# Kernel tuning notes

Hardware: AMD Instinct MI355X
Metric: run time of the kernel (lower is better)

The kernel has to match this reference:

```python
import jax, jax.numpy as jnp
import numpy as np


def setup_inputs() -> dict:
    key = jax.random.key(0)
    kq, kk, kv = jax.random.split(key, 3)
    B, L, Q, H, E = 8, 128, 8, 8, 64
    S, P = 128, 8
    queries = jax.random.normal(kq, (B, L, Q, H, E), dtype=jnp.float32)
    keys = jax.random.normal(kk, (B, S, P, H, E), dtype=jnp.float32)
    values = jax.random.normal(kv, (B, S, P, H, E), dtype=jnp.float32)
    attn_mask = jnp.zeros((1,), dtype=bool)  # unused by the module
    return {"queries": queries, "keys": keys, "values": values, "attn_mask": attn_mask}


def reference(queries, keys, values, attn_mask):
    # queries: [B,L,Q,H,E]; keys/values: [B,S,P,H,E]
    B, L, Q, H, E = queries.shape
    S, P = values.shape[1], values.shape[2]
    scale = 1.0 / np.sqrt(E).astype(np.float32)
    # scores: [B,S,P,L,Q,H]
    scores = jnp.einsum('blqhe,bsphe->bsplqh', queries, keys)
    # softmax over joint (S,P) axis
    scaled = (scale * scores).reshape(B, S * P, L, Q, H)
    attn = jax.nn.softmax(scaled, axis=1).reshape(B, S, P, L, Q, H)
    # dropout is identity in eval / with p=0.0
    V = jnp.einsum('bsphe,bsplqh->blqhe', values, attn)
    return V
```

## Files before the change

kernel.cpp:

```cpp
#include <hip/hip_runtime.h>
#include <hip/hip_bf16.h>

typedef __attribute__((ext_vector_type(4))) float f32x4;
typedef __attribute__((ext_vector_type(16))) float f32x16;
typedef __attribute__((ext_vector_type(8))) short bf16x8;
typedef __attribute__((ext_vector_type(4))) unsigned u32x4;

#define MFMA32(a, b, c) __builtin_amdgcn_mfma_f32_32x32x16_bf16(a, b, c, 0, 0, 0)
#define EXP2(x) __builtin_amdgcn_exp2f(x)

constexpr int Bc = 8, Hc = 8;
constexpr int NQ = 1024;
constexpr int NK = 1024;
constexpr int RS = 512;
constexpr int Ec = 64;
constexpr int KT = 128;
constexpr int NT = NK / KT;
constexpr float QSCALE2 = 0.125f * 1.4426950408889634f;
constexpr float DEFER_THR = 8.0f;

__device__ __forceinline__ short f2bf(float x) {
    return (short)__builtin_bit_cast(unsigned short, __float2bfloat16(x));
}

__device__ __forceinline__ bf16x8 pack2(float4 a, float4 b) {
    bf16x8 r;
    r[0] = f2bf(a.x); r[1] = f2bf(a.y); r[2] = f2bf(a.z); r[3] = f2bf(a.w);
    r[4] = f2bf(b.x); r[5] = f2bf(b.y); r[6] = f2bf(b.z); r[7] = f2bf(b.w);
    return r;
}

__device__ __forceinline__ bf16x8 pack2s(float4 a, float4 b, float s) {
    bf16x8 r;
    r[0] = f2bf(a.x * s); r[1] = f2bf(a.y * s); r[2] = f2bf(a.z * s); r[3] = f2bf(a.w * s);
    r[4] = f2bf(b.x * s); r[5] = f2bf(b.y * s); r[6] = f2bf(b.z * s); r[7] = f2bf(b.w * s);
    return r;
}

__device__ __forceinline__ unsigned cvtpk(float a, float b) {
    unsigned lo = (unsigned short)__builtin_bit_cast(unsigned short, __float2bfloat16(a));
    unsigned hi = (unsigned short)__builtin_bit_cast(unsigned short, __float2bfloat16(b));
    return lo | (hi << 16);
}

__device__ __forceinline__ void gload16(const short* src, short* dst) {
    __builtin_amdgcn_global_load_lds((const __attribute__((address_space(1))) void*)src,
                                     (__attribute__((address_space(3))) void*)dst, 16, 0, 0);
}

__global__ __launch_bounds__(256, 4)
void cvt_kv(const float* __restrict__ Kg, const float* __restrict__ Vg,
            short* __restrict__ Kbf, short* __restrict__ Vt) {
    __shared__ __attribute__((aligned(16))) short Vl[64][72];
    const int tid  = threadIdx.x;
    const int head = blockIdx.x >> 4;
    const int kb   = blockIdx.x & 15;
    const int b    = head >> 3, h = head & 7;
    const int row  = tid >> 2, q = tid & 3;

    const size_t gin = (((size_t)(b * NK + kb * 64 + row)) * 8 + h) * 64 + q * 16;
    const float4* kp = (const float4*)(Kg + gin);
    float4 k0 = kp[0], k1 = kp[1], k2 = kp[2], k3 = kp[3];
    short* kout = Kbf + ((size_t)head * NK + kb * 64 + row) * 64 + q * 16;
    ((bf16x8*)kout)[0] = pack2(k0, k1);
    ((bf16x8*)kout)[1] = pack2(k2, k3);

    const float4* vp = (const float4*)(Vg + gin);
    float4 v0 = vp[0], v1 = vp[1], v2 = vp[2], v3 = vp[3];
    const float vv[16] = {v0.x, v0.y, v0.z, v0.w, v1.x, v1.y, v1.z, v1.w,
                          v2.x, v2.y, v2.z, v2.w, v3.x, v3.y, v3.z, v3.w};
#pragma unroll
    for (int j = 0; j < 16; ++j) Vl[q * 16 + j][row] = f2bf(vv[j]);
    __syncthreads();
    short* vout = Vt + ((size_t)head * Ec + row) * NK + kb * 64 + q * 16;
    ((bf16x8*)vout)[0] = *(const bf16x8*)&Vl[row][q * 16];
    ((bf16x8*)vout)[1] = *(const bf16x8*)&Vl[row][q * 16 + 8];
}

__global__ __launch_bounds__(256, 2)
void fully_attn_kernel(const float* __restrict__ Qg, const short* __restrict__ Kbf,
                       const short* __restrict__ Vt, float* __restrict__ Og) {
    __shared__ __attribute__((aligned(16))) short Kl[2][KT][64];
    __shared__ __attribute__((aligned(16))) short Vl[2][64][KT];

    const int tid  = threadIdx.x;
    const int lane = tid & 63;
    const int wv   = tid >> 6;
    const int ql   = lane & 31;
    const int hi   = lane >> 5;
    const int swz  = (lane & 7) << 4;

    const int bid  = blockIdx.x;
    const int head = (bid & 7) * 8 + (bid >> 6);
    const int qb   = (bid >> 3) & 7;
    const int b    = head >> 3, h = head & 7;

    const size_t headQ = (size_t)b * NQ * RS + (size_t)h * Ec;
    const short* KbfH = Kbf + (size_t)head * NK * Ec;
    const short* VtH  = Vt + (size_t)head * Ec * NK;

    const int qrow = qb * 128 + wv * 32 + ql;
    const float* qp = Qg + headQ + (size_t)qrow * RS;
    bf16x8 qf[4];
#pragma unroll
    for (int j = 0; j < 4; ++j) {
        const float4* q4 = (const float4*)(qp + j * 16 + hi * 8);
        qf[j] = pack2s(q4[0], q4[1], QSCALE2);
    }

    const int klocal = lane >> 3;
    const int kj     = (lane & 7) ^ (klocal & 7);
    const int vlocal = lane >> 4;

#define STAGE(buf, tt)                                                            \
    {                                                                             \
        _Pragma("unroll")                                                         \
        for (int s = 0; s < 4; ++s)                                               \
            gload16(KbfH + (size_t)((tt) * KT + wv * 32 + s * 8 + klocal) * 64 +  \
                        kj * 8,                                                   \
                    &Kl[buf][wv * 32 + s * 8][0]);                                \
        _Pragma("unroll")                                                         \
        for (int s = 0; s < 4; ++s)                                               \
            gload16(VtH + (size_t)(wv * 16 + s * 4 + vlocal) * NK + (tt) * KT +   \
                        (((lane & 15) ^ ((s * 4 + vlocal) & 7)) * 8),             \
                    &Vl[buf][wv * 16 + s * 4][0]);                                \
    }

    STAGE(0, 0);
    __syncthreads();

    float m_r = -1e30f, l_r = 0.0f;
    f32x16 o0 = (f32x16)(0.0f), o1 = (f32x16)(0.0f);

    int cur = 0;
    for (int t = 0; t < NT; ++t) {
        if (t + 1 < NT) STAGE(cur ^ 1, t + 1);

        bf16x8 kf[4][4];
#pragma unroll
        for (int kt = 0; kt < 4; ++kt) {
            const char* kr = (const char*)&Kl[cur][kt * 32 + ql][0];
#pragma unroll
            for (int j = 0; j < 4; ++j)
                kf[kt][j] = *(const bf16x8*)(kr + ((j * 32 + hi * 16) ^ swz));
        }
        f32x16 p[4];
        __builtin_amdgcn_s_setprio(1);
#pragma unroll
        for (int kt = 0; kt < 4; ++kt) {
            f32x16 acc = (f32x16)(0.0f);
#pragma unroll
            for (int j = 0; j < 4; ++j) acc = MFMA32(kf[kt][j], qf[j], acc);
            p[kt] = acc;
        }
        __builtin_amdgcn_s_setprio(0);

        bf16x8 vf0[8], vf1[8];
#pragma unroll
        for (int m = 0; m < 8; ++m) {
            const int cb = (m * 32 + hi * 16) ^ swz;
            vf0[m] = *(const bf16x8*)((const char*)&Vl[cur][ql][0] + cb);
            vf1[m] = *(const bf16x8*)((const char*)&Vl[cur][32 + ql][0] + cb);
        }

        float pm0 = p[0][0], pm1 = p[0][1], pm2 = p[0][2], pm3 = p[0][3];
#pragma unroll
        for (int kt = 0; kt < 4; ++kt)
#pragma unroll
            for (int i = (kt == 0 ? 4 : 0); i < 16; i += 4) {
                pm0 = fmaxf(pm0, p[kt][i + 0]);
                pm1 = fmaxf(pm1, p[kt][i + 1]);
                pm2 = fmaxf(pm2, p[kt][i + 2]);
                pm3 = fmaxf(pm3, p[kt][i + 3]);
            }
        float pm = fmaxf(fmaxf(pm0, pm1), fmaxf(pm2, pm3));
        pm = fmaxf(pm, __shfl_xor(pm, 32));

        if (!__all(pm <= m_r + DEFER_THR)) {
            const float mn = fmaxf(m_r, pm);
            const float alpha = EXP2(m_r - mn);
            l_r *= alpha;
#pragma unroll
            for (int i = 0; i < 16; ++i) { o0[i] *= alpha; o1[i] *= alpha; }
            m_r = mn;
        }

        float rs0 = 0.f, rs1 = 0.f, rs2 = 0.f, rs3 = 0.f;
#pragma unroll
        for (int kt = 0; kt < 4; ++kt)
#pragma unroll
            for (int i = 0; i < 16; i += 4) {
                float e0 = EXP2(p[kt][i + 0] - m_r);
                float e1 = EXP2(p[kt][i + 1] - m_r);
                float e2 = EXP2(p[kt][i + 2] - m_r);
                float e3 = EXP2(p[kt][i + 3] - m_r);
                p[kt][i + 0] = e0; p[kt][i + 1] = e1;
                p[kt][i + 2] = e2; p[kt][i + 3] = e3;
                rs0 += e0; rs1 += e1; rs2 += e2; rs3 += e3;
            }
        l_r += (rs0 + rs1) + (rs2 + rs3);

        __builtin_amdgcn_s_setprio(1);
#pragma unroll
        for (int m = 0; m < 8; ++m) {
            const int kt = m >> 1, r0 = (m & 1) * 8;
            unsigned a0 = cvtpk(p[kt][r0 + 0], p[kt][r0 + 1]);
            unsigned a1 = cvtpk(p[kt][r0 + 2], p[kt][r0 + 3]);
            unsigned b0 = cvtpk(p[kt][r0 + 4], p[kt][r0 + 5]);
            unsigned b1 = cvtpk(p[kt][r0 + 6], p[kt][r0 + 7]);
            asm("v_permlane32_swap_b32 %0, %1" : "+v"(a0), "+v"(b0));
            asm("v_permlane32_swap_b32 %0, %1" : "+v"(a1), "+v"(b1));
            u32x4 w = {a0, a1, b0, b1};
            bf16x8 pf = __builtin_bit_cast(bf16x8, w);
            o0 = MFMA32(vf0[m], pf, o0);
            o1 = MFMA32(vf1[m], pf, o1);
        }
        __builtin_amdgcn_s_setprio(0);

        __syncthreads();
        cur ^= 1;
    }

    l_r += __shfl_xor(l_r, 32);
    const float inv = 1.0f / l_r;
    float* op = Og + headQ + (size_t)qrow * RS;
#pragma unroll
    for (int bnk = 0; bnk < 4; ++bnk) {
        float4 s0 = {o0[bnk * 4 + 0] * inv, o0[bnk * 4 + 1] * inv,
                     o0[bnk * 4 + 2] * inv, o0[bnk * 4 + 3] * inv};
        float4 s1 = {o1[bnk * 4 + 0] * inv, o1[bnk * 4 + 1] * inv,
                     o1[bnk * 4 + 2] * inv, o1[bnk * 4 + 3] * inv};
        *(float4*)(op + bnk * 8 + hi * 4)      = s0;
        *(float4*)(op + 32 + bnk * 8 + hi * 4) = s1;
    }
}

extern "C" void kernel_launch(void* const* d_in, const int* in_sizes, int n_in,
                              void* d_out, int out_size, void* d_ws, size_t ws_size,
                              hipStream_t stream) {
    const float* Qg = (const float*)d_in[0];
    const float* Kg = (const float*)d_in[1];
    const float* Vg = (const float*)d_in[2];
    float* Og = (float*)d_out;

    short* Kbf = (short*)d_ws;
    short* Vt  = (short*)d_ws + (size_t)64 * NK * Ec;

    hipLaunchKernelGGL(cvt_kv, dim3(64 * 16), dim3(256), 0, stream, Kg, Vg, Kbf, Vt);
    hipLaunchKernelGGL(fully_attn_kernel, dim3(512), dim3(256), 0, stream,
                       Qg, Kbf, Vt, Og);
}
```

Before: 44.83 us.

## Split KV range across two wave groups per block and merge softmax states

```diff
diff --git a/kernel.cpp b/kernel.cpp
--- a/kernel.cpp
+++ b/kernel.cpp
@@ -9,13 +9,12 @@
 #define MFMA32(a, b, c) __builtin_amdgcn_mfma_f32_32x32x16_bf16(a, b, c, 0, 0, 0)
 #define EXP2(x) __builtin_amdgcn_exp2f(x)
 
-constexpr int Bc = 8, Hc = 8;
 constexpr int NQ = 1024;
 constexpr int NK = 1024;
 constexpr int RS = 512;
 constexpr int Ec = 64;
-constexpr int KT = 128;
-constexpr int NT = NK / KT;
+constexpr int KT = 64;
+constexpr int NR = 8;
 constexpr float QSCALE2 = 0.125f * 1.4426950408889634f;
 constexpr float DEFER_THR = 8.0f;
 
@@ -77,15 +76,17 @@
     ((bf16x8*)vout)[1] = *(const bf16x8*)&Vl[row][q * 16 + 8];
 }
 
-__global__ __launch_bounds__(256, 2)
+__global__ __launch_bounds__(512, 4)
 void fully_attn_kernel(const float* __restrict__ Qg, const short* __restrict__ Kbf,
                        const short* __restrict__ Vt, float* __restrict__ Og) {
-    __shared__ __attribute__((aligned(16))) short Kl[2][KT][64];
-    __shared__ __attribute__((aligned(16))) short Vl[2][64][KT];
+    __shared__ __attribute__((aligned(16))) short Kl[2][2][64][64];
+    __shared__ __attribute__((aligned(16))) short Vl[2][2][64][64];
 
     const int tid  = threadIdx.x;
     const int lane = tid & 63;
     const int wv   = tid >> 6;
+    const int grp  = wv & 3;
+    const int par  = wv >> 2;
     const int ql   = lane & 31;
     const int hi   = lane >> 5;
     const int swz  = (lane & 7) << 4;
@@ -99,7 +100,7 @@
     const short* KbfH = Kbf + (size_t)head * NK * Ec;
     const short* VtH  = Vt + (size_t)head * Ec * NK;
 
-    const int qrow = qb * 128 + wv * 32 + ql;
+    const int qrow = qb * 128 + grp * 32 + ql;
     const float* qp = Qg + headQ + (size_t)qrow * RS;
     bf16x8 qf[4];
 #pragma unroll
@@ -108,22 +109,19 @@
         qf[j] = pack2s(q4[0], q4[1], QSCALE2);
     }
 
-    const int klocal = lane >> 3;
-    const int kj     = (lane & 7) ^ (klocal & 7);
-    const int vlocal = lane >> 4;
-
-#define STAGE(buf, tt)                                                            \
-    {                                                                             \
-        _Pragma("unroll")                                                         \
-        for (int s = 0; s < 4; ++s)                                               \
-            gload16(KbfH + (size_t)((tt) * KT + wv * 32 + s * 8 + klocal) * 64 +  \
-                        kj * 8,                                                   \
-                    &Kl[buf][wv * 32 + s * 8][0]);                                \
-        _Pragma("unroll")                                                         \
-        for (int s = 0; s < 4; ++s)                                               \
-            gload16(VtH + (size_t)(wv * 16 + s * 4 + vlocal) * NK + (tt) * KT +   \
-                        (((lane & 15) ^ ((s * 4 + vlocal) & 7)) * 8),             \
-                    &Vl[buf][wv * 16 + s * 4][0]);                                \
+    const int srow = wv * 8 + (lane >> 3);
+    const int sj   = (lane & 7) ^ ((lane >> 3) & 7);
+
+#define STAGE(buf, rr)                                                           \
+    {                                                                            \
+        gload16(KbfH + (size_t)((2 * (rr)) * KT + srow) * 64 + sj * 8,           \
+                &Kl[buf][0][wv * 8][0]);                                         \
+        gload16(KbfH + (size_t)((2 * (rr) + 1) * KT + srow) * 64 + sj * 8,       \
+                &Kl[buf][1][wv * 8][0]);                                         \
+        gload16(VtH + (size_t)srow * NK + (2 * (rr)) * KT + sj * 8,              \
+                &Vl[buf][0][wv * 8][0]);                                         \
+        gload16(VtH + (size_t)srow * NK + (2 * (rr) + 1) * KT + sj * 8,          \
+                &Vl[buf][1][wv * 8][0]);                                         \
     }
 
     STAGE(0, 0);
@@ -133,21 +131,21 @@
     f32x16 o0 = (f32x16)(0.0f), o1 = (f32x16)(0.0f);
 
     int cur = 0;
-    for (int t = 0; t < NT; ++t) {
-        if (t + 1 < NT) STAGE(cur ^ 1, t + 1);
-
-        bf16x8 kf[4][4];
-#pragma unroll
-        for (int kt = 0; kt < 4; ++kt) {
-            const char* kr = (const char*)&Kl[cur][kt * 32 + ql][0];
+    for (int r = 0; r < NR; ++r) {
+        if (r + 1 < NR) STAGE(cur ^ 1, r + 1);
+
+        bf16x8 kf[2][4];
+#pragma unroll
+        for (int kt = 0; kt < 2; ++kt) {
+            const char* kr = (const char*)&Kl[cur][par][kt * 32 + ql][0];
 #pragma unroll
             for (int j = 0; j < 4; ++j)
                 kf[kt][j] = *(const bf16x8*)(kr + ((j * 32 + hi * 16) ^ swz));
         }
-        f32x16 p[4];
+        f32x16 p[2];
         __builtin_amdgcn_s_setprio(1);
 #pragma unroll
-        for (int kt = 0; kt < 4; ++kt) {
+        for (int kt = 0; kt < 2; ++kt) {
             f32x16 acc = (f32x16)(0.0f);
 #pragma unroll
             for (int j = 0; j < 4; ++j) acc = MFMA32(kf[kt][j], qf[j], acc);
@@ -155,17 +153,17 @@
         }
         __builtin_amdgcn_s_setprio(0);
 
-        bf16x8 vf0[8], vf1[8];
-#pragma unroll
-        for (int m = 0; m < 8; ++m) {
+        bf16x8 vf0[4], vf1[4];
+#pragma unroll
+        for (int m = 0; m < 4; ++m) {
             const int cb = (m * 32 + hi * 16) ^ swz;
-            vf0[m] = *(const bf16x8*)((const char*)&Vl[cur][ql][0] + cb);
-            vf1[m] = *(const bf16x8*)((const char*)&Vl[cur][32 + ql][0] + cb);
+            vf0[m] = *(const bf16x8*)((const char*)&Vl[cur][par][ql][0] + cb);
+            vf1[m] = *(const bf16x8*)((const char*)&Vl[cur][par][32 + ql][0] + cb);
         }
 
         float pm0 = p[0][0], pm1 = p[0][1], pm2 = p[0][2], pm3 = p[0][3];
 #pragma unroll
-        for (int kt = 0; kt < 4; ++kt)
+        for (int kt = 0; kt < 2; ++kt)
 #pragma unroll
             for (int i = (kt == 0 ? 4 : 0); i < 16; i += 4) {
                 pm0 = fmaxf(pm0, p[kt][i + 0]);
@@ -187,7 +185,7 @@
 
         float rs0 = 0.f, rs1 = 0.f, rs2 = 0.f, rs3 = 0.f;
 #pragma unroll
-        for (int kt = 0; kt < 4; ++kt)
+        for (int kt = 0; kt < 2; ++kt)
 #pragma unroll
             for (int i = 0; i < 16; i += 4) {
                 float e0 = EXP2(p[kt][i + 0] - m_r);
@@ -202,7 +200,7 @@
 
         __builtin_amdgcn_s_setprio(1);
 #pragma unroll
-        for (int m = 0; m < 8; ++m) {
+        for (int m = 0; m < 4; ++m) {
             const int kt = m >> 1, r0 = (m & 1) * 8;
             unsigned a0 = cvtpk(p[kt][r0 + 0], p[kt][r0 + 1]);
             unsigned a1 = cvtpk(p[kt][r0 + 2], p[kt][r0 + 3]);
@@ -222,16 +220,41 @@
     }
 
     l_r += __shfl_xor(l_r, 32);
-    const float inv = 1.0f / l_r;
-    float* op = Og + headQ + (size_t)qrow * RS;
-#pragma unroll
-    for (int bnk = 0; bnk < 4; ++bnk) {
-        float4 s0 = {o0[bnk * 4 + 0] * inv, o0[bnk * 4 + 1] * inv,
-                     o0[bnk * 4 + 2] * inv, o0[bnk * 4 + 3] * inv};
-        float4 s1 = {o1[bnk * 4 + 0] * inv, o1[bnk * 4 + 1] * inv,
-                     o1[bnk * 4 + 2] * inv, o1[bnk * 4 + 3] * inv};
-        *(float4*)(op + bnk * 8 + hi * 4)      = s0;
-        *(float4*)(op + 32 + bnk * 8 + hi * 4) = s1;
+
+    float* scrO  = (float*)&Kl[0][0][0][0];
+    float* scrML = (float*)&Vl[0][0][0][0];
+    const int slot = grp * 64 + lane;
+    if (par == 1) {
+#pragma unroll
+        for (int i = 0; i < 16; ++i) {
+            scrO[i * 256 + slot]         = o0[i];
+            scrO[(16 + i) * 256 + slot]  = o1[i];
+        }
+        scrML[slot * 2 + 0] = m_r;
+        scrML[slot * 2 + 1] = l_r;
+    }
+    __syncthreads();
+    if (par == 0) {
+        const float m_b = scrML[slot * 2 + 0];
+        const float l_b = scrML[slot * 2 + 1];
+        const float M  = fmaxf(m_r, m_b);
+        const float aa = EXP2(m_r - M);
+        const float ab = EXP2(m_b - M);
+        const float inv = 1.0f / (aa * l_r + ab * l_b);
+
+        float* op = Og + headQ + (size_t)qrow * RS;
+#pragma unroll
+        for (int bnk = 0; bnk < 4; ++bnk) {
+            float4 s0, s1;
+#pragma unroll
+            for (int j = 0; j < 4; ++j) {
+                const int i = bnk * 4 + j;
+                ((float*)&s0)[j] = (aa * o0[i] + ab * scrO[i * 256 + slot]) * inv;
+                ((float*)&s1)[j] = (aa * o1[i] + ab * scrO[(16 + i) * 256 + slot]) * inv;
+            }
+            *(float4*)(op + bnk * 8 + hi * 4)      = s0;
+            *(float4*)(op + 32 + bnk * 8 + hi * 4) = s1;
+        }
     }
 }
 
@@ -247,6 +270,6 @@
     short* Vt  = (short*)d_ws + (size_t)64 * NK * Ec;
 
     hipLaunchKernelGGL(cvt_kv, dim3(64 * 16), dim3(256), 0, stream, Kg, Vg, Kbf, Vt);
-    hipLaunchKernelGGL(fully_attn_kernel, dim3(512), dim3(256), 0, stream,
+    hipLaunchKernelGGL(fully_attn_kernel, dim3(512), dim3(512), 0, stream,
                        Qg, Kbf, Vt, Og);
 }
```

Result: slower. 51.73 us (+15.4%).
